# Kernel optimization log

Hardware: AMD Instinct MI355X
Metric: run time of the kernel (lower is better)

Reference implementation:

```python
import jax, jax.numpy as jnp
import numpy as np

EPS = 1e-5

def activation_quant(x):
    # per-token absmax int8 quantization (fake-quant, STE)
    scale = 127.0 / jnp.clip(jnp.max(jnp.abs(x), axis=-1, keepdims=True), EPS, None)
    xq = jnp.clip(jnp.round(x * scale), -128.0, 127.0) / scale
    return x + jax.lax.stop_gradient(xq - x)

def weight_quant(w):
    # per-tensor ternary quantization with mean-abs scale (BitNet b1.58)
    scale = 1.0 / jnp.clip(jnp.mean(jnp.abs(w)), EPS, None)
    wq = jnp.clip(jnp.round(w * scale), -1.0, 1.0) / scale
    return w + jax.lax.stop_gradient(wq - w)

def bitlinear(x, w):
    # w: [out, in]; y = x_q @ w_q^T
    return jnp.einsum('bsd,od->bso', activation_quant(x), weight_quant(w))

def setup_inputs() -> dict:
    key = jax.random.key(0)
    k1, k2, k3 = jax.random.split(key, 3)
    dim, inner = 2048, 8192
    x = jax.random.normal(k1, (4, 2048, dim), dtype=jnp.float32)
    w1 = jax.random.normal(k2, (inner, dim), dtype=jnp.float32) * (dim ** -0.5)
    w2 = jax.random.normal(k3, (dim, inner), dtype=jnp.float32) * (inner ** -0.5)
    return {"x": x, "w1": w1, "w2": w2}

def reference(x, w1, w2):
    h = bitlinear(x, w1)          # [B, S, inner]
    h = jax.nn.relu(h)
    return bitlinear(h, w2)       # [B, S, dim]
```

## Files before the change

### kernel.cpp

```cpp
#include <hip/hip_runtime.h>
#include <hip/hip_bf16.h>
#include <stdint.h>

#define EPSQ 1e-5f

typedef int i32x4 __attribute__((ext_vector_type(4)));

__device__ inline void gload16(const void* g, void* l){
  __builtin_amdgcn_global_load_lds((const __attribute__((address_space(1))) unsigned int*)g,
                                   (__attribute__((address_space(3))) unsigned int*)l, 16, 0, 0);
}

__device__ inline unsigned pack4(float4 v, float s, float lo, float hi){
  int a = (int)fminf(fmaxf(rintf(v.x*s), lo), hi);
  int b = (int)fminf(fmaxf(rintf(v.y*s), lo), hi);
  int c = (int)fminf(fmaxf(rintf(v.z*s), lo), hi);
  int d = (int)fminf(fmaxf(rintf(v.w*s), lo), hi);
  return (unsigned)((a&255)|((b&255)<<8)|((c&255)<<16)|((d&255)<<24));
}

__global__ void absmean2(const float* __restrict__ w1, const float* __restrict__ w2,
                         int n4, double* __restrict__ partial){
  const int half = blockIdx.x >> 10;
  const float4* w4 = (const float4*)(half ? w2 : w1);
  double s = 0.0;
  int idx = (blockIdx.x & 1023)*blockDim.x + threadIdx.x;
  int stride = 1024*blockDim.x;
  for (int i = idx; i < n4; i += stride){
    float4 v = w4[i];
    s += (double)(fabsf(v.x)+fabsf(v.y)+fabsf(v.z)+fabsf(v.w));
  }
  __shared__ double sm[256];
  sm[threadIdx.x] = s; __syncthreads();
  for (int o=128;o>0;o>>=1){ if (threadIdx.x<o) sm[threadIdx.x]+=sm[threadIdx.x+o]; __syncthreads(); }
  if (threadIdx.x==0) partial[blockIdx.x] = sm[0];
}

__global__ void finalize_scales(const double* __restrict__ partial, float* __restrict__ scalebuf, double inv_n){
  __shared__ double sm[256];
  int t = threadIdx.x;
  double s1 = partial[t] + partial[t+256] + partial[t+512] + partial[t+768];
  sm[t]=s1; __syncthreads();
  for(int o=128;o>0;o>>=1){ if(t<o) sm[t]+=sm[t+o]; __syncthreads(); }
  double m1 = sm[0];
  __syncthreads();
  double s2 = partial[1024+t]+partial[1280+t]+partial[1536+t]+partial[1792+t];
  sm[t]=s2; __syncthreads();
  for(int o=128;o>0;o>>=1){ if(t<o) sm[t]+=sm[t+o]; __syncthreads(); }
  if (t==0){
    scalebuf[0] = 1.0f / fmaxf((float)(m1*inv_n),    EPSQ);
    scalebuf[1] = 1.0f / fmaxf((float)(sm[0]*inv_n), EPSQ);
  }
}

__global__ void wquant8(const float* __restrict__ w, char* __restrict__ wq,
                        const float* __restrict__ scalebuf, int which){
  int i = blockIdx.x*256 + threadIdx.x;
  float s = scalebuf[which];
  const float4* w4 = (const float4*)w;
  float4 v0 = w4[(size_t)i*4], v1 = w4[(size_t)i*4+1], v2 = w4[(size_t)i*4+2], v3 = w4[(size_t)i*4+3];
  uint4 pk = make_uint4(pack4(v0,s,-1.f,1.f), pack4(v1,s,-1.f,1.f),
                        pack4(v2,s,-1.f,1.f), pack4(v3,s,-1.f,1.f));
  *reinterpret_cast<uint4*>(wq + (size_t)i*16) = pk;
}

__global__ void aquant8c(const float* __restrict__ x, char* __restrict__ xq,
                         float* __restrict__ s_a, int* __restrict__ rowMax){
  int m = blockIdx.x, t = threadIdx.x;
  if (t==0) rowMax[m] = 0;
  const float4* x4 = (const float4*)(x + (size_t)m*2048);
  float4 a = x4[t*2], b = x4[t*2+1];
  float va[8] = {a.x,a.y,a.z,a.w,b.x,b.y,b.z,b.w};
  float mx = 0.f;
  #pragma unroll
  for (int j=0;j<8;j++) mx = fmaxf(mx, fabsf(va[j]));
  #pragma unroll
  for (int o=1;o<64;o<<=1) mx = fmaxf(mx, __shfl_xor(mx, o, 64));
  __shared__ float wm[4];
  if ((t&63)==0) wm[t>>6] = mx;
  __syncthreads();
  mx = fmaxf(fmaxf(wm[0],wm[1]), fmaxf(wm[2],wm[3]));
  float s = 127.f / fmaxf(mx, EPSQ);
  if (t==0) s_a[m] = s;
  uint2 pk = make_uint2(pack4(a,s,-128.f,127.f), pack4(b,s,-128.f,127.f));
  *reinterpret_cast<uint2*>(xq + (size_t)m*2048 + t*8) = pk;
}

template<int EPI, int STEPS>
__global__ __launch_bounds__(256,2) void gemmK(
    const char* __restrict__ A, const char* __restrict__ B, void* __restrict__ Cv,
    int moff, int* __restrict__ rowMax, const float* __restrict__ s_a,
    const float* __restrict__ scalebuf)
{
  const int Ks = STEPS << 7;
  __shared__ __align__(16) char sm[2*32768 + 1024];
  int* smax = (int*)(sm + 2*32768);
  const int tid = threadIdx.x, lane = tid & 63, w = tid >> 6;
  const int wr = w >> 1, wc = w & 1;
  const int n0 = blockIdx.x*128, m0 = blockIdx.y*128;

  i32x4 acc[4][4] = {};

  const int trow = tid >> 3;
  const int scl  = (tid & 7) ^ (trow & 7);
  const char* gA = A + (size_t)(m0 + trow)*Ks + scl*16;
  const char* gB = B + (size_t)(n0 + trow)*Ks + scl*16;

  auto stage = [&](int sbase, int kt){
    #pragma unroll
    for (int i=0;i<4;i++){
      gload16(gA + kt + (size_t)(i*32)*Ks, sm + sbase + (i*256+tid)*16);
      gload16(gB + kt + (size_t)(i*32)*Ks, sm + sbase + 16384 + (i*256+tid)*16);
    }
  };

  const int frow = lane & 15, kb = lane >> 4;
  int aoff[2][4], boff[2][4];
  #pragma unroll
  for (int kh=0;kh<2;kh++){
    #pragma unroll
    for (int f=0;f<4;f++){
      int ra = wr*64 + f*16 + frow;
      aoff[kh][f] = ra*128 + ((((kh<<2)|kb) ^ (ra&7))<<4);
      int rb = wc*64 + f*16 + frow;
      boff[kh][f] = 16384 + rb*128 + ((((kh<<2)|kb) ^ (rb&7))<<4);
    }
  }

  auto kstep = [&](const int slot, int t, const int mode){
    const char* base = sm + slot*32768;
    i32x4 av0[4], bv0[4], av1[4], bv1[4];
    #pragma unroll
    for (int f=0;f<4;f++){
      av0[f] = *reinterpret_cast<const i32x4*>(base + aoff[0][f]);
      bv0[f] = *reinterpret_cast<const i32x4*>(base + boff[0][f]);
    }
    #pragma unroll
    for (int f=0;f<4;f++){
      av1[f] = *reinterpret_cast<const i32x4*>(base + aoff[1][f]);
      bv1[f] = *reinterpret_cast<const i32x4*>(base + boff[1][f]);
    }
    if (mode == 0) stage((slot^1)*32768, (t+1)<<7);
    asm volatile("s_waitcnt lgkmcnt(8)" ::: "memory");
    __builtin_amdgcn_sched_barrier(0);
    __builtin_amdgcn_s_setprio(1);
    #pragma unroll
    for (int fm=0;fm<4;fm++)
      #pragma unroll
      for (int fn=0;fn<4;fn++)
        acc[fm][fn] = __builtin_amdgcn_mfma_i32_16x16x64_i8(av0[fm], bv0[fn], acc[fm][fn], 0,0,0);
    __builtin_amdgcn_s_setprio(0);
    asm volatile("s_waitcnt lgkmcnt(0)" ::: "memory");
    __builtin_amdgcn_sched_barrier(0);
    __builtin_amdgcn_s_setprio(1);
    #pragma unroll
    for (int fm=0;fm<4;fm++)
      #pragma unroll
      for (int fn=0;fn<4;fn++)
        acc[fm][fn] = __builtin_amdgcn_mfma_i32_16x16x64_i8(av1[fm], bv1[fn], acc[fm][fn], 0,0,0);
    __builtin_amdgcn_s_setprio(0);
    if (mode == 0) asm volatile("s_waitcnt vmcnt(0)" ::: "memory");
    if (mode != 2) __builtin_amdgcn_s_barrier();
  };

  stage(0, 0);
  asm volatile("s_waitcnt vmcnt(0)" ::: "memory");
  __builtin_amdgcn_s_barrier();
  __builtin_amdgcn_sched_barrier(0);

  for (int tt = 0; tt < STEPS/2 - 1; ++tt){
    int t = tt*2;
    kstep(0, t,   0);
    kstep(1, t+1, 0);
  }
  kstep(0, STEPS-2, 0);
  kstep(1, STEPS-1, 2);

  const int cc = lane & 15, cr = (lane >> 4)*4;
  if (EPI == 0){
    __syncthreads();
    if (tid < 128) smax[tid] = 0;
    __syncthreads();
    ushort* C16 = (ushort*)Cv;
    #pragma unroll
    for (int fm=0;fm<4;fm++){
      #pragma unroll
      for (int reg=0;reg<4;reg++){
        int rl = wr*64 + fm*16 + cr + reg;
        size_t r = (size_t)(m0 + rl);
        int rmax = 0;
        #pragma unroll
        for (int fn=0;fn<4;fn++){
          int v = acc[fm][fn][reg]; v = v > 0 ? v : 0;
          C16[r*8192 + n0 + wc*64 + fn*16 + cc] = (ushort)(v > 65535 ? 65535 : v);
          rmax = v > rmax ? v : rmax;
        }
        atomicMax(&smax[rl], rmax);
      }
    }
    __syncthreads();
    if (tid < 128) atomicMax(&rowMax[m0 + tid], smax[tid]);
  } else {
    float* out = (float*)Cv;
    float sw1 = scalebuf[0], sw2 = scalebuf[1];
    #pragma unroll
    for (int fm=0;fm<4;fm++){
      #pragma unroll
      for (int reg=0;reg<4;reg++){
        int rl = wr*64 + fm*16 + cr + reg;
        size_t r = (size_t)(moff + m0 + rl);
        int Mi = rowMax[r];
        float maxref = (float)Mi / (s_a[r]*sw1);
        float inv2 = fmaxf(maxref, EPSQ) / (127.f*sw2);
        #pragma unroll
        for (int fn=0;fn<4;fn++)
          out[r*2048 + n0 + wc*64 + fn*16 + cc] = (float)acc[fm][fn][reg] * inv2;
      }
    }
  }
}

__global__ void hquant(const ushort* __restrict__ h16, char* __restrict__ hq,
                       const int* __restrict__ rowMax){
  int m = blockIdx.y;
  int Mi = rowMax[m];
  float rqv = (Mi > 0) ? 127.f/(float)Mi : 0.f;
  size_t base = (size_t)m*8192 + blockIdx.x*2048 + threadIdx.x*8;
  uint4 pk = *reinterpret_cast<const uint4*>(h16 + base);
  unsigned u[4] = {pk.x, pk.y, pk.z, pk.w};
  unsigned o[2] = {0,0};
  #pragma unroll
  for (int j=0;j<8;j++){
    float h = (float)(u[j>>1] >> ((j&1)*16) & 0xffff);
    int q = (int)fminf(rintf(h*rqv), 127.f);
    o[j>>2] |= (unsigned)(q & 255) << ((j&3)*8);
  }
  *reinterpret_cast<uint2*>(hq + base) = make_uint2(o[0], o[1]);
}

extern "C" void kernel_launch(void* const* d_in, const int* in_sizes, int n_in,
                              void* d_out, int out_size, void* d_ws, size_t ws_size,
                              hipStream_t stream){
  const float* x  = (const float*)d_in[0];
  const float* w1 = (const float*)d_in[1];
  const float* w2 = (const float*)d_in[2];
  float* out = (float*)d_out;

  const int MTOK = 8192, Mc = 1024;
  const size_t nW = (size_t)8192*2048;

  char* ws = (char*)d_ws; size_t off = 0;
  auto alloc = [&](size_t n)->char*{ char* p = ws+off; off = (off+n+255) & ~(size_t)255; return p; };

  float*  s_a     = (float*)alloc((size_t)MTOK*4);
  int*    rowMax  = (int*)  alloc((size_t)MTOK*4);
  float*  scalebuf= (float*)alloc(256);
  double* partial = (double*)alloc(2048*8);
  char*   w1q     = alloc(nW);
  char*   shared  = alloc(nW);
  char*   a8c     = alloc((size_t)Mc*2048);
  ushort* h16     = (ushort*)shared;

  int hqM = 0;
  for (int m = 4096; m >= 1024; m >>= 1)
    if (off + (size_t)m*8192 <= ws_size){ hqM = m; break; }
  if (!hqM) return;
  char* hq = alloc((size_t)hqM*8192);

  absmean2<<<2048,256,0,stream>>>(w1, w2, (int)(nW/4), partial);
  finalize_scales<<<1,256,0,stream>>>(partial, scalebuf, 1.0/(double)nW);
  wquant8<<<(int)(nW/16/256),256,0,stream>>>(w1, w1q, scalebuf, 0);

  for (int s = 0; s < MTOK/hqM; ++s){
    for (int c = 0; c < hqM/Mc; ++c){
      int ch = s*hqM + c*Mc;
      aquant8c<<<Mc,256,0,stream>>>(x + (size_t)ch*2048, a8c, s_a + ch, rowMax + ch);
      gemmK<0,16><<<dim3(64, Mc/128),256,0,stream>>>(
          a8c, w1q, h16, 0, rowMax + ch, nullptr, scalebuf);
      hquant<<<dim3(4, Mc),256,0,stream>>>(h16, hq + (size_t)c*Mc*8192, rowMax + ch);
    }
    wquant8<<<(int)(nW/16/256),256,0,stream>>>(w2, shared, scalebuf, 1);
    gemmK<1,64><<<dim3(16, hqM/128),256,0,stream>>>(
        hq, shared, out, s*hqM, rowMax, s_a, scalebuf);
  }
}
```

Measured before the change: 424.2 us.

## Triple-buffer A tiles with prefetch distance two in int8 GEMM pipeline

Splits LDS staging into separate A and B buffers, with A in three slots prefetched two k-steps ahead and B double-buffered one step ahead. The per-step wait drops from vmcnt(0) to vmcnt(4), so the A loads for the step after next can still be in flight at the barrier. This is meant to hide more global-load latency. In exchange LDS per block grows to 80 KB and the loop is unrolled by six, which requires (STEPS-4) to be divisible by 6 and may limit occupancy.

```diff
diff --git a/kernel.cpp b/kernel.cpp
--- a/kernel.cpp
+++ b/kernel.cpp
@@ -93,8 +93,7 @@
     const float* __restrict__ scalebuf)
 {
   const int Ks = STEPS << 7;
-  __shared__ __align__(16) char sm[2*32768 + 1024];
-  int* smax = (int*)(sm + 2*32768);
+  __shared__ __align__(16) char sm[81920];
   const int tid = threadIdx.x, lane = tid & 63, w = tid >> 6;
   const int wr = w >> 1, wc = w & 1;
   const int n0 = blockIdx.x*128, m0 = blockIdx.y*128;
@@ -106,12 +105,17 @@
   const char* gA = A + (size_t)(m0 + trow)*Ks + scl*16;
   const char* gB = B + (size_t)(n0 + trow)*Ks + scl*16;
 
-  auto stage = [&](int sbase, int kt){
-    #pragma unroll
-    for (int i=0;i<4;i++){
-      gload16(gA + kt + (size_t)(i*32)*Ks, sm + sbase + (i*256+tid)*16);
-      gload16(gB + kt + (size_t)(i*32)*Ks, sm + sbase + 16384 + (i*256+tid)*16);
-    }
+  auto stA = [&](const int slot, int t){
+    int kt = t << 7;
+    #pragma unroll
+    for (int i=0;i<4;i++)
+      gload16(gA + kt + (size_t)(i*32)*Ks, sm + slot*16384 + (i*256+tid)*16);
+  };
+  auto stB = [&](const int slot, int t){
+    int kt = t << 7;
+    #pragma unroll
+    for (int i=0;i<4;i++)
+      gload16(gB + kt + (size_t)(i*32)*Ks, sm + 49152 + slot*16384 + (i*256+tid)*16);
   };
 
   const int frow = lane & 15, kb = lane >> 4;
@@ -123,24 +127,26 @@
       int ra = wr*64 + f*16 + frow;
       aoff[kh][f] = ra*128 + ((((kh<<2)|kb) ^ (ra&7))<<4);
       int rb = wc*64 + f*16 + frow;
-      boff[kh][f] = 16384 + rb*128 + ((((kh<<2)|kb) ^ (rb&7))<<4);
-    }
-  }
-
-  auto kstep = [&](const int slot, int t, const int mode){
-    const char* base = sm + slot*32768;
+      boff[kh][f] = rb*128 + ((((kh<<2)|kb) ^ (rb&7))<<4);
+    }
+  }
+
+  auto kstep = [&](const int sA, const int sB, int t, const int mode){
+    const char* baseA = sm + sA*16384;
+    const char* baseB = sm + 49152 + sB*16384;
+    if (mode == 0){ stB(sB^1, t+1); stA((sA+2>=3)?sA-1:sA+2, t+2); }
+    else if (mode == 1){ stB(sB^1, t+1); }
     i32x4 av0[4], bv0[4], av1[4], bv1[4];
     #pragma unroll
     for (int f=0;f<4;f++){
-      av0[f] = *reinterpret_cast<const i32x4*>(base + aoff[0][f]);
-      bv0[f] = *reinterpret_cast<const i32x4*>(base + boff[0][f]);
+      av0[f] = *reinterpret_cast<const i32x4*>(baseA + aoff[0][f]);
+      bv0[f] = *reinterpret_cast<const i32x4*>(baseB + boff[0][f]);
     }
     #pragma unroll
     for (int f=0;f<4;f++){
-      av1[f] = *reinterpret_cast<const i32x4*>(base + aoff[1][f]);
-      bv1[f] = *reinterpret_cast<const i32x4*>(base + boff[1][f]);
-    }
-    if (mode == 0) stage((slot^1)*32768, (t+1)<<7);
+      av1[f] = *reinterpret_cast<const i32x4*>(baseA + aoff[1][f]);
+      bv1[f] = *reinterpret_cast<const i32x4*>(baseB + boff[1][f]);
+    }
     asm volatile("s_waitcnt lgkmcnt(8)" ::: "memory");
     __builtin_amdgcn_sched_barrier(0);
     __builtin_amdgcn_s_setprio(1);
@@ -159,23 +165,27 @@
       for (int fn=0;fn<4;fn++)
         acc[fm][fn] = __builtin_amdgcn_mfma_i32_16x16x64_i8(av1[fm], bv1[fn], acc[fm][fn], 0,0,0);
     __builtin_amdgcn_s_setprio(0);
-    if (mode == 0) asm volatile("s_waitcnt vmcnt(0)" ::: "memory");
+    if (mode == 0)      asm volatile("s_waitcnt vmcnt(4)" ::: "memory");
+    else if (mode == 1) asm volatile("s_waitcnt vmcnt(0)" ::: "memory");
     if (mode != 2) __builtin_amdgcn_s_barrier();
   };
 
-  stage(0, 0);
-  asm volatile("s_waitcnt vmcnt(0)" ::: "memory");
+  stB(0, 0); stA(0, 0); stA(1, 1);
+  asm volatile("s_waitcnt vmcnt(4)" ::: "memory");
   __builtin_amdgcn_s_barrier();
   __builtin_amdgcn_sched_barrier(0);
 
-  for (int tt = 0; tt < STEPS/2 - 1; ++tt){
-    int t = tt*2;
-    kstep(0, t,   0);
-    kstep(1, t+1, 0);
-  }
-  kstep(0, STEPS-2, 0);
-  kstep(1, STEPS-1, 2);
-
+  for (int tt = 0; tt < (STEPS-4)/6; ++tt){
+    int t = tt*6;
+    kstep(0,0,t,  0); kstep(1,1,t+1,0); kstep(2,0,t+2,0);
+    kstep(0,1,t+3,0); kstep(1,0,t+4,0); kstep(2,1,t+5,0);
+  }
+  kstep(0,0,STEPS-4,0);
+  kstep(1,1,STEPS-3,0);
+  kstep(2,0,STEPS-2,1);
+  kstep(0,1,STEPS-1,2);
+
+  int* smax = (int*)sm;
   const int cc = lane & 15, cr = (lane >> 4)*4;
   if (EPI == 0){
     __syncthreads();
```

Result: no change. 429.8 us (+1.3%).

## Fuse hidden requantization into GEMM1 via grid-wide spin barrier, batch weight quant

Applied to the files above, without the earlier changes.

GEMM1 now computes per-row ReLU maxima, waits at a grid-wide atomic-counter spin barrier for all 512 blocks, then requantizes its accumulator tile to int8 in registers and writes it straight to the hidden buffer. This removes the uint16 intermediate write, the separate hquant pass and its reread. Both weight matrices are quantized in one launch, and activation quantization runs once up front when workspace allows. The spin barrier assumes all 512 blocks are co-resident (two per CU on 256 CUs), and its bounded spin budget can silently fall through if they are not.

```diff
diff --git a/kernel.cpp b/kernel.cpp
--- a/kernel.cpp
+++ b/kernel.cpp
@@ -53,10 +53,14 @@
   }
 }
 
-__global__ void wquant8(const float* __restrict__ w, char* __restrict__ wq,
-                        const float* __restrict__ scalebuf, int which){
+__global__ void wquant2(const float* __restrict__ w1, const float* __restrict__ w2,
+                        char* __restrict__ q1, char* __restrict__ q2,
+                        const float* __restrict__ scalebuf){
+  int which = blockIdx.y;
+  const float* w = which ? w2 : w1;
+  char* wq = which ? q2 : q1;
+  float s = scalebuf[which];
   int i = blockIdx.x*256 + threadIdx.x;
-  float s = scalebuf[which];
   const float4* w4 = (const float4*)w;
   float4 v0 = w4[(size_t)i*4], v1 = w4[(size_t)i*4+1], v2 = w4[(size_t)i*4+2], v3 = w4[(size_t)i*4+3];
   uint4 pk = make_uint4(pack4(v0,s,-1.f,1.f), pack4(v1,s,-1.f,1.f),
@@ -86,13 +90,12 @@
   *reinterpret_cast<uint2*>(xq + (size_t)m*2048 + t*8) = pk;
 }
 
-template<int EPI, int STEPS>
-__global__ __launch_bounds__(256,2) void gemmK(
-    const char* __restrict__ A, const char* __restrict__ B, void* __restrict__ Cv,
-    int moff, int* __restrict__ rowMax, const float* __restrict__ s_a,
-    const float* __restrict__ scalebuf)
+__global__ __launch_bounds__(256,2) void gemm1swb(
+    const char* __restrict__ A, const char* __restrict__ B, char* __restrict__ hq,
+    int* __restrict__ rowMax, int* __restrict__ ctr)
 {
-  const int Ks = STEPS << 7;
+  constexpr int STEPS = 16;
+  const int Ks = 2048;
   __shared__ __align__(16) char sm[2*32768 + 1024];
   int* smax = (int*)(sm + 2*32768);
   const int tid = threadIdx.x, lane = tid & 63, w = tid >> 6;
@@ -177,65 +180,167 @@
   kstep(1, STEPS-1, 2);
 
   const int cc = lane & 15, cr = (lane >> 4)*4;
-  if (EPI == 0){
-    __syncthreads();
-    if (tid < 128) smax[tid] = 0;
-    __syncthreads();
-    ushort* C16 = (ushort*)Cv;
-    #pragma unroll
-    for (int fm=0;fm<4;fm++){
-      #pragma unroll
-      for (int reg=0;reg<4;reg++){
-        int rl = wr*64 + fm*16 + cr + reg;
-        size_t r = (size_t)(m0 + rl);
-        int rmax = 0;
-        #pragma unroll
-        for (int fn=0;fn<4;fn++){
-          int v = acc[fm][fn][reg]; v = v > 0 ? v : 0;
-          C16[r*8192 + n0 + wc*64 + fn*16 + cc] = (ushort)(v > 65535 ? 65535 : v);
-          rmax = v > rmax ? v : rmax;
-        }
-        atomicMax(&smax[rl], rmax);
+  __syncthreads();
+  if (tid < 128) smax[tid] = 0;
+  __syncthreads();
+  #pragma unroll
+  for (int fm=0;fm<4;fm++){
+    #pragma unroll
+    for (int reg=0;reg<4;reg++){
+      int rl = wr*64 + fm*16 + cr + reg;
+      int rmax = 0;
+      #pragma unroll
+      for (int fn=0;fn<4;fn++){
+        int v = acc[fm][fn][reg]; v = v > 0 ? v : 0;
+        acc[fm][fn][reg] = v;
+        rmax = v > rmax ? v : rmax;
       }
-    }
-    __syncthreads();
-    if (tid < 128) atomicMax(&rowMax[m0 + tid], smax[tid]);
-  } else {
-    float* out = (float*)Cv;
-    float sw1 = scalebuf[0], sw2 = scalebuf[1];
-    #pragma unroll
-    for (int fm=0;fm<4;fm++){
-      #pragma unroll
-      for (int reg=0;reg<4;reg++){
-        int rl = wr*64 + fm*16 + cr + reg;
-        size_t r = (size_t)(moff + m0 + rl);
-        int Mi = rowMax[r];
-        float maxref = (float)Mi / (s_a[r]*sw1);
-        float inv2 = fmaxf(maxref, EPSQ) / (127.f*sw2);
-        #pragma unroll
-        for (int fn=0;fn<4;fn++)
-          out[r*2048 + n0 + wc*64 + fn*16 + cc] = (float)acc[fm][fn][reg] * inv2;
+      atomicMax(&smax[rl], rmax);
+    }
+  }
+  __syncthreads();
+  if (tid < 128) atomicMax(&rowMax[m0 + tid], smax[tid]);
+  __syncthreads();
+
+  if (tid == 0){
+    __threadfence();
+    atomicAdd(ctr, 1);
+    int budget = 1 << 22;
+    while (atomicAdd(ctr, 0) < 512 && --budget) {}
+  }
+  __syncthreads();
+
+  if (tid < 128) smax[tid] = atomicAdd(&rowMax[m0 + tid], 0);
+  __syncthreads();
+  #pragma unroll
+  for (int fm=0;fm<4;fm++){
+    #pragma unroll
+    for (int reg=0;reg<4;reg++){
+      int rl = wr*64 + fm*16 + cr + reg;
+      int Mi = smax[rl];
+      float rqv = (Mi > 0) ? 127.f/(float)Mi : 0.f;
+      #pragma unroll
+      for (int fn=0;fn<4;fn++){
+        int q = (int)fminf(rintf((float)acc[fm][fn][reg]*rqv), 127.f);
+        sm[rl*128 + wc*64 + fn*16 + cc] = (char)q;
       }
     }
   }
-}
-
-__global__ void hquant(const ushort* __restrict__ h16, char* __restrict__ hq,
-                       const int* __restrict__ rowMax){
-  int m = blockIdx.y;
-  int Mi = rowMax[m];
-  float rqv = (Mi > 0) ? 127.f/(float)Mi : 0.f;
-  size_t base = (size_t)m*8192 + blockIdx.x*2048 + threadIdx.x*8;
-  uint4 pk = *reinterpret_cast<const uint4*>(h16 + base);
-  unsigned u[4] = {pk.x, pk.y, pk.z, pk.w};
-  unsigned o[2] = {0,0};
-  #pragma unroll
-  for (int j=0;j<8;j++){
-    float h = (float)(u[j>>1] >> ((j&1)*16) & 0xffff);
-    int q = (int)fminf(rintf(h*rqv), 127.f);
-    o[j>>2] |= (unsigned)(q & 255) << ((j&3)*8);
-  }
-  *reinterpret_cast<uint2*>(hq + base) = make_uint2(o[0], o[1]);
+  __syncthreads();
+  {
+    const uint4* src = (const uint4*)(sm + tid*64);
+    char* dst = hq + (size_t)(m0 + (tid>>1))*8192 + n0 + (tid&1)*64;
+    #pragma unroll
+    for (int i=0;i<4;i++)
+      *reinterpret_cast<uint4*>(dst + i*16) = src[i];
+  }
+}
+
+template<int STEPS>
+__global__ __launch_bounds__(256,2) void gemm2K(
+    const char* __restrict__ A, const char* __restrict__ B, float* __restrict__ out,
+    int moff, const int* __restrict__ rowMax, const float* __restrict__ s_a,
+    const float* __restrict__ scalebuf)
+{
+  const int Ks = STEPS << 7;
+  __shared__ __align__(16) char sm[2*32768 + 1024];
+  const int tid = threadIdx.x, lane = tid & 63, w = tid >> 6;
+  const int wr = w >> 1, wc = w & 1;
+  const int n0 = blockIdx.x*128, m0 = blockIdx.y*128;
+
+  i32x4 acc[4][4] = {};
+
+  const int trow = tid >> 3;
+  const int scl  = (tid & 7) ^ (trow & 7);
+  const char* gA = A + (size_t)(m0 + trow)*Ks + scl*16;
+  const char* gB = B + (size_t)(n0 + trow)*Ks + scl*16;
+
+  auto stage = [&](int sbase, int kt){
+    #pragma unroll
+    for (int i=0;i<4;i++){
+      gload16(gA + kt + (size_t)(i*32)*Ks, sm + sbase + (i*256+tid)*16);
+      gload16(gB + kt + (size_t)(i*32)*Ks, sm + sbase + 16384 + (i*256+tid)*16);
+    }
+  };
+
+  const int frow = lane & 15, kb = lane >> 4;
+  int aoff[2][4], boff[2][4];
+  #pragma unroll
+  for (int kh=0;kh<2;kh++){
+    #pragma unroll
+    for (int f=0;f<4;f++){
+      int ra = wr*64 + f*16 + frow;
+      aoff[kh][f] = ra*128 + ((((kh<<2)|kb) ^ (ra&7))<<4);
+      int rb = wc*64 + f*16 + frow;
+      boff[kh][f] = 16384 + rb*128 + ((((kh<<2)|kb) ^ (rb&7))<<4);
+    }
+  }
+
+  auto kstep = [&](const int slot, int t, const int mode){
+    const char* base = sm + slot*32768;
+    i32x4 av0[4], bv0[4], av1[4], bv1[4];
+    #pragma unroll
+    for (int f=0;f<4;f++){
+      av0[f] = *reinterpret_cast<const i32x4*>(base + aoff[0][f]);
+      bv0[f] = *reinterpret_cast<const i32x4*>(base + boff[0][f]);
+    }
+    #pragma unroll
+    for (int f=0;f<4;f++){
+      av1[f] = *reinterpret_cast<const i32x4*>(base + aoff[1][f]);
+      bv1[f] = *reinterpret_cast<const i32x4*>(base + boff[1][f]);
+    }
+    if (mode == 0) stage((slot^1)*32768, (t+1)<<7);
+    asm volatile("s_waitcnt lgkmcnt(8)" ::: "memory");
+    __builtin_amdgcn_sched_barrier(0);
+    __builtin_amdgcn_s_setprio(1);
+    #pragma unroll
+    for (int fm=0;fm<4;fm++)
+      #pragma unroll
+      for (int fn=0;fn<4;fn++)
+        acc[fm][fn] = __builtin_amdgcn_mfma_i32_16x16x64_i8(av0[fm], bv0[fn], acc[fm][fn], 0,0,0);
+    __builtin_amdgcn_s_setprio(0);
+    asm volatile("s_waitcnt lgkmcnt(0)" ::: "memory");
+    __builtin_amdgcn_sched_barrier(0);
+    __builtin_amdgcn_s_setprio(1);
+    #pragma unroll
+    for (int fm=0;fm<4;fm++)
+      #pragma unroll
+      for (int fn=0;fn<4;fn++)
+        acc[fm][fn] = __builtin_amdgcn_mfma_i32_16x16x64_i8(av1[fm], bv1[fn], acc[fm][fn], 0,0,0);
+    __builtin_amdgcn_s_setprio(0);
+    if (mode == 0) asm volatile("s_waitcnt vmcnt(0)" ::: "memory");
+    if (mode != 2) __builtin_amdgcn_s_barrier();
+  };
+
+  stage(0, 0);
+  asm volatile("s_waitcnt vmcnt(0)" ::: "memory");
+  __builtin_amdgcn_s_barrier();
+  __builtin_amdgcn_sched_barrier(0);
+
+  for (int tt = 0; tt < STEPS/2 - 1; ++tt){
+    int t = tt*2;
+    kstep(0, t,   0);
+    kstep(1, t+1, 0);
+  }
+  kstep(0, STEPS-2, 0);
+  kstep(1, STEPS-1, 2);
+
+  const int cc = lane & 15, cr = (lane >> 4)*4;
+  float sw1 = scalebuf[0], sw2 = scalebuf[1];
+  #pragma unroll
+  for (int fm=0;fm<4;fm++){
+    #pragma unroll
+    for (int reg=0;reg<4;reg++){
+      int rl = wr*64 + fm*16 + cr + reg;
+      size_t r = (size_t)(moff + m0 + rl);
+      int Mi = rowMax[r];
+      float maxref = (float)Mi / (s_a[r]*sw1);
+      float inv2 = fmaxf(maxref, EPSQ) / (127.f*sw2);
+      #pragma unroll
+      for (int fn=0;fn<4;fn++)
+        out[r*2048 + n0 + wc*64 + fn*16 + cc] = (float)acc[fm][fn][reg] * inv2;
+    }
+  }
 }
 
 extern "C" void kernel_launch(void* const* d_in, const int* in_sizes, int n_in,
@@ -246,7 +351,7 @@
   const float* w2 = (const float*)d_in[2];
   float* out = (float*)d_out;
 
-  const int MTOK = 8192, Mc = 1024;
+  const int MTOK = 8192, Mc = 1024, hqM = 4096;
   const size_t nW = (size_t)8192*2048;
 
   char* ws = (char*)d_ws; size_t off = 0;
@@ -256,31 +361,40 @@
   int*    rowMax  = (int*)  alloc((size_t)MTOK*4);
   float*  scalebuf= (float*)alloc(256);
   double* partial = (double*)alloc(2048*8);
+  int*    ctrs    = (int*)  alloc(64);
   char*   w1q     = alloc(nW);
-  char*   shared  = alloc(nW);
-  char*   a8c     = alloc((size_t)Mc*2048);
-  ushort* h16     = (ushort*)shared;
-
-  int hqM = 0;
-  for (int m = 4096; m >= 1024; m >>= 1)
-    if (off + (size_t)m*8192 <= ws_size){ hqM = m; break; }
-  if (!hqM) return;
-  char* hq = alloc((size_t)hqM*8192);
-
+  char*   w2q     = alloc(nW);
+
+  bool fullA = false;
+  char *a8 = nullptr, *hq = nullptr;
+  if (off + nW  + 2*nW  + 4096 <= ws_size){
+    fullA = true;
+    a8 = alloc(nW);
+    hq = alloc(2*nW);
+  } else if (off + (size_t)Mc*2048 + 2*nW + 4096 <= ws_size){
+    a8 = alloc((size_t)Mc*2048);
+    hq = alloc(2*nW);
+  } else return;
+
+  hipMemsetAsync(ctrs, 0, 64, stream);
   absmean2<<<2048,256,0,stream>>>(w1, w2, (int)(nW/4), partial);
   finalize_scales<<<1,256,0,stream>>>(partial, scalebuf, 1.0/(double)nW);
-  wquant8<<<(int)(nW/16/256),256,0,stream>>>(w1, w1q, scalebuf, 0);
+  wquant2<<<dim3((int)(nW/16/256),2),256,0,stream>>>(w1, w2, w1q, w2q, scalebuf);
+  if (fullA) aquant8c<<<MTOK,256,0,stream>>>(x, a8, s_a, rowMax);
 
   for (int s = 0; s < MTOK/hqM; ++s){
     for (int c = 0; c < hqM/Mc; ++c){
       int ch = s*hqM + c*Mc;
-      aquant8c<<<Mc,256,0,stream>>>(x + (size_t)ch*2048, a8c, s_a + ch, rowMax + ch);
-      gemmK<0,16><<<dim3(64, Mc/128),256,0,stream>>>(
-          a8c, w1q, h16, 0, rowMax + ch, nullptr, scalebuf);
-      hquant<<<dim3(4, Mc),256,0,stream>>>(h16, hq + (size_t)c*Mc*8192, rowMax + ch);
-    }
-    wquant8<<<(int)(nW/16/256),256,0,stream>>>(w2, shared, scalebuf, 1);
-    gemmK<1,64><<<dim3(16, hqM/128),256,0,stream>>>(
-        hq, shared, out, s*hqM, rowMax, s_a, scalebuf);
-  }
-}
+      const char* aptr;
+      if (fullA) aptr = a8 + (size_t)ch*2048;
+      else {
+        aquant8c<<<Mc,256,0,stream>>>(x + (size_t)ch*2048, a8, s_a + ch, rowMax + ch);
+        aptr = a8;
+      }
+      gemm1swb<<<dim3(64, Mc/128),256,0,stream>>>(
+          aptr, w1q, hq + (size_t)c*Mc*8192, rowMax + ch, ctrs + (s*4 + c));
+    }
+    gemm2K<64><<<dim3(16, hqM/128),256,0,stream>>>(
+        hq, w2q, out, s*hqM, rowMax, s_a, scalebuf);
+  }
+}
```

Result: slower. 538.8 us (+27.0%).

## Add 256x256-tile int8 GEMM1 kernel and larger chunking when workspace allows

Applied to the files above, without the earlier changes.

Adds a 512-thread GEMM1 kernel with 256x256 output tiles and 128 KB of double-buffered LDS, which raises operand reuse per LDS load and halves the number of blocks. When the workspace is large enough, activations are quantized in a single launch, and both GEMMs run on bigger chunks (Mc=2048, hqM=4096), so fewer kernels are launched and w2 is requantized fewer times. The large LDS footprint may cap occupancy at one block per CU despite the launch bound of 2, and the small-workspace path keeps the old code.

```diff
diff --git a/kernel.cpp b/kernel.cpp
--- a/kernel.cpp
+++ b/kernel.cpp
@@ -86,6 +86,109 @@
   *reinterpret_cast<uint2*>(xq + (size_t)m*2048 + t*8) = pk;
 }
 
+__global__ __launch_bounds__(512,2) void gemm1_256(
+    const char* __restrict__ A, const char* __restrict__ B, ushort* __restrict__ C16,
+    int* __restrict__ rowMax)
+{
+  constexpr int STEPS = 16;
+  const int Ks = 2048;
+  __shared__ __align__(16) char sm[2*65536 + 1024];
+  int* smax = (int*)(sm + 2*65536);
+  const int tid = threadIdx.x, lane = tid & 63, w = tid >> 6;
+  const int wr = w >> 1, wc = w & 1;
+  const int n0 = blockIdx.x*256, m0 = blockIdx.y*256;
+
+  i32x4 acc[4][8] = {};
+
+  const int trow = tid >> 3;
+  const int scl  = (tid & 7) ^ (trow & 7);
+  const char* gA = A + (size_t)(m0 + trow)*Ks + scl*16;
+  const char* gB = B + (size_t)(n0 + trow)*Ks + scl*16;
+
+  auto stage = [&](int sbase, int kt){
+    #pragma unroll
+    for (int i=0;i<4;i++)
+      gload16(gA + kt + (size_t)(i*64)*Ks, sm + sbase + (i*512+tid)*16);
+    #pragma unroll
+    for (int i=0;i<4;i++)
+      gload16(gB + kt + (size_t)(i*64)*Ks, sm + sbase + 32768 + (i*512+tid)*16);
+  };
+
+  const int frow = lane & 15, kb = lane >> 4;
+  int aoff[2][4], boff[2][8];
+  #pragma unroll
+  for (int kh=0;kh<2;kh++){
+    #pragma unroll
+    for (int f=0;f<4;f++){
+      int ra = wr*64 + f*16 + frow;
+      aoff[kh][f] = ra*128 + ((((kh<<2)|kb) ^ (ra&7))<<4);
+    }
+    #pragma unroll
+    for (int f=0;f<8;f++){
+      int rb = wc*128 + f*16 + frow;
+      boff[kh][f] = 32768 + rb*128 + ((((kh<<2)|kb) ^ (rb&7))<<4);
+    }
+  }
+
+  auto kstep = [&](const int slot, int t, const int mode){
+    const char* base = sm + slot*65536;
+    if (mode == 0) stage((slot^1)*65536, (t+1)<<7);
+    #pragma unroll
+    for (int kh=0;kh<2;kh++){
+      i32x4 av[4], bv[8];
+      #pragma unroll
+      for (int f=0;f<4;f++) av[f] = *reinterpret_cast<const i32x4*>(base + aoff[kh][f]);
+      #pragma unroll
+      for (int f=0;f<8;f++) bv[f] = *reinterpret_cast<const i32x4*>(base + boff[kh][f]);
+      __builtin_amdgcn_s_setprio(1);
+      #pragma unroll
+      for (int fm=0;fm<4;fm++)
+        #pragma unroll
+        for (int fn=0;fn<8;fn++)
+          acc[fm][fn] = __builtin_amdgcn_mfma_i32_16x16x64_i8(av[fm], bv[fn], acc[fm][fn], 0,0,0);
+      __builtin_amdgcn_s_setprio(0);
+    }
+    if (mode == 0) asm volatile("s_waitcnt vmcnt(0)" ::: "memory");
+    if (mode != 2) __builtin_amdgcn_s_barrier();
+  };
+
+  stage(0, 0);
+  asm volatile("s_waitcnt vmcnt(0)" ::: "memory");
+  __builtin_amdgcn_s_barrier();
+  __builtin_amdgcn_sched_barrier(0);
+
+  for (int tt = 0; tt < STEPS/2 - 1; ++tt){
+    int t = tt*2;
+    kstep(0, t,   0);
+    kstep(1, t+1, 0);
+  }
+  kstep(0, STEPS-2, 0);
+  kstep(1, STEPS-1, 2);
+
+  const int cc = lane & 15, cr = (lane >> 4)*4;
+  __syncthreads();
+  if (tid < 256) smax[tid] = 0;
+  __syncthreads();
+  #pragma unroll
+  for (int fm=0;fm<4;fm++){
+    #pragma unroll
+    for (int reg=0;reg<4;reg++){
+      int rl = wr*64 + fm*16 + cr + reg;
+      size_t r = (size_t)(m0 + rl);
+      int rmax = 0;
+      #pragma unroll
+      for (int fn=0;fn<8;fn++){
+        int v = acc[fm][fn][reg]; v = v > 0 ? v : 0;
+        C16[r*8192 + n0 + wc*128 + fn*16 + cc] = (ushort)(v > 65535 ? 65535 : v);
+        rmax = v > rmax ? v : rmax;
+      }
+      atomicMax(&smax[rl], rmax);
+    }
+  }
+  __syncthreads();
+  if (tid < 256) atomicMax(&rowMax[m0 + tid], smax[tid]);
+}
+
 template<int EPI, int STEPS>
 __global__ __launch_bounds__(256,2) void gemmK(
     const char* __restrict__ A, const char* __restrict__ B, void* __restrict__ Cv,
@@ -246,7 +349,7 @@
   const float* w2 = (const float*)d_in[2];
   float* out = (float*)d_out;
 
-  const int MTOK = 8192, Mc = 1024;
+  const int MTOK = 8192;
   const size_t nW = (size_t)8192*2048;
 
   char* ws = (char*)d_ws; size_t off = 0;
@@ -257,30 +360,48 @@
   float*  scalebuf= (float*)alloc(256);
   double* partial = (double*)alloc(2048*8);
   char*   w1q     = alloc(nW);
-  char*   shared  = alloc(nW);
-  char*   a8c     = alloc((size_t)Mc*2048);
-  ushort* h16     = (ushort*)shared;
-
-  int hqM = 0;
-  for (int m = 4096; m >= 1024; m >>= 1)
-    if (off + (size_t)m*8192 <= ws_size){ hqM = m; break; }
-  if (!hqM) return;
-  char* hq = alloc((size_t)hqM*8192);
+
+  bool big = false;
+  char *w2q=nullptr, *a8=nullptr, *hq=nullptr;
+  ushort* h16=nullptr;
+  int hqM = 4096, Mc = 2048;
+  if (off + 2*nW  + nW  + 2*nW  + 4096 <= ws_size){
+    big = true;
+    h16 = (ushort*)alloc(2*nW);
+    w2q = (char*)h16;
+    a8  = alloc(nW);
+    hq  = alloc(2*nW);
+  } else {
+    Mc = 1024;
+    h16 = (ushort*)alloc(nW); w2q = (char*)h16;
+    a8  = alloc((size_t)Mc*2048);
+    hqM = 0;
+    for (int m = 4096; m >= 1024; m >>= 1)
+      if (off + (size_t)m*8192 <= ws_size){ hqM = m; break; }
+    if (!hqM) return;
+    hq = alloc((size_t)hqM*8192);
+  }
 
   absmean2<<<2048,256,0,stream>>>(w1, w2, (int)(nW/4), partial);
   finalize_scales<<<1,256,0,stream>>>(partial, scalebuf, 1.0/(double)nW);
   wquant8<<<(int)(nW/16/256),256,0,stream>>>(w1, w1q, scalebuf, 0);
+  if (big) aquant8c<<<MTOK,256,0,stream>>>(x, a8, s_a, rowMax);
 
   for (int s = 0; s < MTOK/hqM; ++s){
     for (int c = 0; c < hqM/Mc; ++c){
       int ch = s*hqM + c*Mc;
-      aquant8c<<<Mc,256,0,stream>>>(x + (size_t)ch*2048, a8c, s_a + ch, rowMax + ch);
-      gemmK<0,16><<<dim3(64, Mc/128),256,0,stream>>>(
-          a8c, w1q, h16, 0, rowMax + ch, nullptr, scalebuf);
+      if (big){
+        gemm1_256<<<dim3(32, Mc/256),512,0,stream>>>(
+            a8 + (size_t)ch*2048, w1q, h16, rowMax + ch);
+      } else {
+        aquant8c<<<Mc,256,0,stream>>>(x + (size_t)ch*2048, a8, s_a + ch, rowMax + ch);
+        gemmK<0,16><<<dim3(64, Mc/128),256,0,stream>>>(
+            a8, w1q, h16, 0, rowMax + ch, nullptr, scalebuf);
+      }
       hquant<<<dim3(4, Mc),256,0,stream>>>(h16, hq + (size_t)c*Mc*8192, rowMax + ch);
     }
-    wquant8<<<(int)(nW/16/256),256,0,stream>>>(w2, shared, scalebuf, 1);
+    wquant8<<<(int)(nW/16/256),256,0,stream>>>(w2, w2q, scalebuf, 1);
     gemmK<1,64><<<dim3(16, hqM/128),256,0,stream>>>(
-        hq, shared, out, s*hqM, rowMax, s_a, scalebuf);
-  }
-}
+        hq, w2q, out, s*hqM, rowMax, s_a, scalebuf);
+  }
+}
```

After: 363.9 us, median of 2. 14.2% less time.
